# Performance work log

Hardware: AMD Instinct MI355X
Metric: run time of the kernel (lower is better)

## Reference

```python
import jax, jax.numpy as jnp
from jax import lax
import numpy as np


def _tv1d_row(y, lam):
    """Condat's direct O(n) 1D TV-L1 prox (TV1D_denoise) on one row.
    Solves min_x 0.5*||x-y||^2 + lam * sum|x_{i+1}-x_i|.
    State machine translation of Condat (2013) Algorithm 1.
    """
    W = y.shape[0]
    idx = jnp.arange(W)
    dt = y.dtype

    def write(out, lo, hi, v):
        # out[lo:hi+1] = v  (masked, jit-friendly)
        return jnp.where((idx >= lo) & (idx <= hi), v, out)

    def cond_fn(s):
        return ~s[9]

    def body_fn(s):
        out, k, k0, km, kp, umin, umax, vmin, vmax, done = s
        T = jnp.array(True)
        F = jnp.array(False)

        def branchA(_):  # k == W-1
            def a1(_):  # umin < 0: flush negative segment at vmin
                o = write(out, k0, km, vmin)
                k0n = km + 1
                vminn = y[jnp.minimum(k0n, W - 1)]
                return (o, k0n, k0n, k0n, kp, lam, vminn + lam - vmax, vminn, vmax, F)

            def a2(_):  # umax > 0: flush positive segment at vmax
                o = write(out, k0, kp, vmax)
                k0n = kp + 1
                vmaxn = y[jnp.minimum(k0n, W - 1)]
                return (o, k0n, k0n, km, k0n, vmaxn - lam - vmin, -lam, vmin, vmaxn, F)

            def a3(_):  # terminate
                v = vmin + umin / (k - k0 + 1).astype(dt)
                o = write(out, k0, k, v)
                return (o, k, k0, km, kp, umin, umax, v, vmax, T)

            return lax.cond(umin < 0, a1,
                            lambda _: lax.cond(umax > 0, a2, a3, None), None)

        def branchB(_):  # k < W-1
            yn = y[jnp.minimum(k + 1, W - 1)]
            umin_t = umin + yn - vmin
            umax_t = umax + yn - vmax

            def b1(_):  # negative jump: flush at vmin, restart
                o = write(out, k0, km, vmin)
                k0n = km + 1
                vminn = y[jnp.minimum(k0n, W - 1)]
                return (o, k0n, k0n, k0n, k0n, lam, -lam, vminn, vminn + 2 * lam, F)

            def b2(_):  # positive jump: flush at vmax, restart
                o = write(out, k0, kp, vmax)
                k0n = kp + 1
                vmaxn = y[jnp.minimum(k0n, W - 1)]
                return (o, k0n, k0n, k0n, k0n, lam, -lam, vmaxn - 2 * lam, vmaxn, F)

            def b3(_):  # extend current segment
                kn = k + 1
                denom = (kn - k0 + 1).astype(dt)
                hit_min = umin_t >= lam
                hit_max = umax_t <= -lam
                vminn = jnp.where(hit_min, vmin + (umin_t - lam) / denom, vmin)
                uminn = jnp.where(hit_min, lam, umin_t)
                kmn = jnp.where(hit_min, kn, km)
                vmaxn = jnp.where(hit_max, vmax + (umax_t + lam) / denom, vmax)
                umaxn = jnp.where(hit_max, -lam, umax_t)
                kpn = jnp.where(hit_max, kn, kp)
                return (out, kn, k0, kmn, kpn, uminn, umaxn, vminn, vmaxn, F)

            return lax.cond(umin_t < -lam, b1,
                            lambda _: lax.cond(umax_t > lam, b2, b3, None), None)

        return lax.cond(k == W - 1, branchA, branchB, None)

    z = jnp.int32(0)
    init = (jnp.zeros_like(y), z, z, z, z, lam, -lam, y[0] - lam, y[0] + lam, jnp.array(False))
    return lax.while_loop(cond_fn, body_fn, init)[0]


def tv1d_batch(y_flat, lam_rows):
    return jax.vmap(_tv1d_row)(y_flat, lam_rows)


def setup_inputs() -> dict:
    key = jax.random.key(0)
    N, C, H, W = 8, 3, 256, 512
    y = jax.random.normal(key, (N, C, H, W), dtype=jnp.float32)
    # learned lmbd parameter initialized so that softplus(lmbd) = 0.5 (lmbd_init=0.5, lmbd_zero<0 -> offset 0)
    lmbd = jnp.full((1, C), float(np.log(np.expm1(0.5))), dtype=jnp.float32)
    return {"y": y, "lmbd": lmbd}


def reference(y, lmbd):
    N, C, H, W = y.shape
    lam = jax.nn.softplus(lmbd)  # get_lmbd_val with lmbd_offset = 0
    lam_rows = jnp.broadcast_to(lam.reshape(1, C, 1), (N, C, H)).reshape(-1)  # (N*C*H,)
    x = tv1d_batch(y.reshape(-1, W), lam_rows)
    return x.reshape(N, C, H, W)
```

## Files before the change

### kernel.cpp

```cpp
#include <hip/hip_runtime.h>
#include <math.h>

#define TVW 512
#define TVH 256
#define TVC 3
#define WPB 2
#define BLOCK (WPB * 64)
#define PAD 12
#define RTN 528

__global__ __launch_bounds__(BLOCK)
void tv1d_condat_wave_kernel(const float* __restrict__ y,
                             const float* __restrict__ lmbd,
                             float* __restrict__ out,
                             int total_rows) {
    __shared__ __align__(16) float buf [WPB * TVW + PAD];
    __shared__ __align__(16) float bneg[WPB * TVW + PAD];
    __shared__ __align__(16) float rtab[RTN];
    const int tid  = threadIdx.x;
    const int wave = tid >> 6;
    const int lane = tid & 63;
    const int l32  = lane & 31;
    const bool hi  = lane >= 32;
    const int row  = blockIdx.x * WPB + wave;

    if (row < total_rows) {
        const float4* s4 = (const float4*)(y + (size_t)row * TVW);
        float4* b4 = (float4*)(buf  + wave * TVW);
        float4* n4 = (float4*)(bneg + wave * TVW);
        #pragma unroll
        for (int i = 0; i < TVW / 4; i += 64) {
            const float4 vv = s4[i + lane];
            b4[i + lane] = vv;
            n4[i + lane] = make_float4(-vv.x, -vv.y, -vv.z, -vv.w);
        }
    }
    if (tid < PAD) {
        buf [WPB * TVW + tid] = 0.0f;
        bneg[WPB * TVW + tid] = 0.0f;
    }
    for (int i = tid; i < RTN; i += BLOCK)
        rtab[i] = 1.0f / (float)(i == 0 ? 1 : i);
    __syncthreads();

    if (row < total_rows) {
        const int c = (row / TVH) % TVC;
        float lam = log1pf(expf(lmbd[c]));
        lam = __uint_as_float(__builtin_amdgcn_readfirstlane(__float_as_uint(lam)));
        const float nlam   = -lam;
        const float twolam = 2.0f * lam;
        float* x = buf + wave * TVW;
        const float* xs = hi ? (bneg + wave * TVW) : (buf + wave * TVW);
        const float cneg = hi ? twolam : 0.0f;
        const float cpos = hi ? 0.0f : twolam;

        int k0, t, trips, rem, seg_guard;
        int kmv, kcv;
        unsigned long long jb;
        float u, v, nv, tt, wv, den_f;
        float P0, P1, P2, P3, Q0, Q1, Q2, Q3, R0, R1, R2, R3, e0, e1, e2;
        float2 TAr, TBr, TAp, TBp, TAq, TBq;
        const float* rt;
        bool negj;

        k0 = 0; seg_guard = 2048; jb = 0;
        kmv = 0; kcv = 1;
        v = xs[0] - lam;
        u = lam;
        P0 = xs[1];  P1 = xs[2];  P2 = xs[3];  P3 = xs[4];
        Q0 = xs[5];  Q1 = xs[6];  Q2 = xs[7];  Q3 = xs[8];
        R0 = xs[9];  R1 = xs[10]; R2 = xs[11]; R3 = xs[12];

#define TVSTEP(EV, RN) { \
            const float u_t = u + (EV) - v; \
            jb = __ballot(u_t < nlam);    \
            if (jb) goto midjump; \
            kmv = (u_t >= lam) ? kcv : kmv;   \
            kcv += 1; \
            const float u_n = fminf(u_t, lam); \
            v = fmaf(u_t - u_n, (RN), v);   \
            u = u_n; }

#define TVPHASE(B0_, B1_, B2_, B3_, TA_, TB_) { \
            TVSTEP(B0_, TA_.x) \
            TVSTEP(B1_, TA_.y) \
            TVSTEP(B2_, TB_.x) \
            TVSTEP(B3_, TB_.y) \
            B0_ = xs[k0 + t + 13]; B1_ = xs[k0 + t + 14]; \
            B2_ = xs[k0 + t + 15]; B3_ = xs[k0 + t + 16]; \
            TA_ = *(const float2*)(rt + 12); \
            TB_ = *(const float2*)(rt + 14); \
            rt += 4; t += 4; }

seg_start:
        if (--seg_guard < 0) goto done;
        trips = (TVW - 1) - k0;
        TAr = *(const float2*)(rtab + 10); TBr = *(const float2*)(rtab + 12);
        TAp = *(const float2*)(rtab + 14); TBp = *(const float2*)(rtab + 16);
        TAq = *(const float2*)(rtab + 18); TBq = *(const float2*)(rtab + 20);
        if (trips < 4) { t = 0; e0 = P0; e1 = P1; e2 = P2; goto rem_steps; }
        TVSTEP(P0, 0.5f)
        TVSTEP(P1, (1.0f / 3.0f))
        TVSTEP(P2, 0.25f)
        TVSTEP(P3, 0.2f)
        P0 = xs[k0 + 13]; P1 = xs[k0 + 14]; P2 = xs[k0 + 15]; P3 = xs[k0 + 16];
        if (trips < 8) { t = 4; e0 = Q0; e1 = Q1; e2 = Q2; goto rem_steps; }
        TVSTEP(Q0, (1.0f / 6.0f))
        TVSTEP(Q1, (1.0f / 7.0f))
        TVSTEP(Q2, 0.125f)
        TVSTEP(Q3, (1.0f / 9.0f))
        Q0 = xs[k0 + 17]; Q1 = xs[k0 + 18]; Q2 = xs[k0 + 19]; Q3 = xs[k0 + 20];
        t = 8;
        rt = rtab + 10;
        for (;;) {
            if (t + 4 > trips) { e0 = R0; e1 = R1; e2 = R2; break; }
            TVPHASE(R0, R1, R2, R3, TAr, TBr)
            if (t + 4 > trips) { e0 = P0; e1 = P1; e2 = P2; break; }
            TVPHASE(P0, P1, P2, P3, TAp, TBp)
            if (t + 4 > trips) { e0 = Q0; e1 = Q1; e2 = Q2; break; }
            TVPHASE(Q0, Q1, Q2, Q3, TAq, TBq)
        }
rem_steps:
        rem = trips - t;
        if (rem > 0) {
            den_f = (float)(t + 2);
            TVSTEP(e0, __builtin_amdgcn_rcpf(den_f))
            if (rem > 1) {
                TVSTEP(e1, __builtin_amdgcn_rcpf(den_f + 1.0f))
                if (rem > 2) {
                    TVSTEP(e2, __builtin_amdgcn_rcpf(den_f + 2.0f))
                }
            }
        }

        {
            const unsigned long long bb = __ballot(u < 0.0f);
            if ((unsigned)bb) {
                const int fe = __builtin_amdgcn_readlane(kmv, 0);
                const int k0n = fe + 1;
                wv = v;
                if (k0n < TVW) {
                    nv = xs[k0n];
                    P0 = xs[k0n + 1];  P1 = xs[k0n + 2];  P2 = xs[k0n + 3];  P3 = xs[k0n + 4];
                    Q0 = xs[k0n + 5];  Q1 = xs[k0n + 6];  Q2 = xs[k0n + 7];  Q3 = xs[k0n + 8];
                    R0 = xs[k0n + 9];  R1 = xs[k0n + 10]; R2 = xs[k0n + 11]; R3 = xs[k0n + 12];
                }
                { const int pe = fe < TVW - 1 ? fe : TVW - 1;
                  if (!hi) for (int p = k0 + l32; p <= pe; p += 32) x[p] = wv; }
                if (k0n >= TVW) goto done;
                tt = nv - lam;
                u = hi ? (tt - v) : lam;
                v = hi ? v : nv;
                k0 = k0n;
                kmv = hi ? kmv : k0n;
                kcv = k0n + 1;
                goto seg_start;
            } else if ((unsigned)(bb >> 32)) {
                const int fe = __builtin_amdgcn_readlane(kmv, 32);
                const int k0n = fe + 1;
                wv = -v;
                if (k0n < TVW) {
                    nv = xs[k0n];
                    P0 = xs[k0n + 1];  P1 = xs[k0n + 2];  P2 = xs[k0n + 3];  P3 = xs[k0n + 4];
                    Q0 = xs[k0n + 5];  Q1 = xs[k0n + 6];  Q2 = xs[k0n + 7];  Q3 = xs[k0n + 8];
                    R0 = xs[k0n + 9];  R1 = xs[k0n + 10]; R2 = xs[k0n + 11]; R3 = xs[k0n + 12];
                }
                { const int pe = fe < TVW - 1 ? fe : TVW - 1;
                  if (hi) for (int p = k0 + l32; p <= pe; p += 32) x[p] = wv; }
                if (k0n >= TVW) goto done;
                tt = nv - lam;
                u = hi ? lam : (tt - v);
                v = hi ? nv : v;
                k0 = k0n;
                kmv = hi ? k0n : kmv;
                kcv = k0n + 1;
                goto seg_start;
            } else {
                const float vt = fmaf(u, __builtin_amdgcn_rcpf((float)(trips + 1)), v);
                if (!hi) for (int p = k0 + l32; p < TVW; p += 32) x[p] = vt;
                goto done;
            }
        }

midjump:
        {
            negj = (unsigned)jb != 0;
            const int fe = __builtin_amdgcn_readlane(kmv, negj ? 0 : 32);
            const int k0n = fe + 1;
            wv = hi ? -v : v;
            nv = xs[k0n];
            P0 = xs[k0n + 1];  P1 = xs[k0n + 2];  P2 = xs[k0n + 3];  P3 = xs[k0n + 4];
            Q0 = xs[k0n + 5];  Q1 = xs[k0n + 6];  Q2 = xs[k0n + 7];  Q3 = xs[k0n + 8];
            R0 = xs[k0n + 9];  R1 = xs[k0n + 10]; R2 = xs[k0n + 11]; R3 = xs[k0n + 12];
            {
                const int p0 = k0 + l32;
                if ((negj != hi) && (p0 <= fe)) x[p0] = wv;
                if (fe - k0 >= 32) {
                    if (negj != hi)
                        for (int p = p0 + 32; p <= fe; p += 32) x[p] = wv;
                }
            }
            k0 = k0n;
            kmv = k0n; kcv = k0n + 1;
            v = nv - (negj ? cneg : cpos);
            u = lam;
            goto seg_start;
        }
#undef TVPHASE
#undef TVSTEP
done:   ;
        {
            const float4* b4 = (const float4*)(buf + wave * TVW);
            float4* d4 = (float4*)(out + (size_t)row * TVW);
            #pragma unroll
            for (int i = 0; i < TVW / 4; i += 64)
                d4[i + lane] = b4[i + lane];
        }
    }
}

extern "C" void kernel_launch(void* const* d_in, const int* in_sizes, int n_in,
                              void* d_out, int out_size, void* d_ws, size_t ws_size,
                              hipStream_t stream) {
    const float* y    = (const float*)d_in[0];
    const float* lmbd = (const float*)d_in[1];
    float* out = (float*)d_out;

    const int total_rows = in_sizes[0] / TVW;
    const int grid = (total_rows + WPB - 1) / WPB;
    tv1d_condat_wave_kernel<<<grid, BLOCK, 0, stream>>>(y, lmbd, out, total_rows);
}
```

Baseline: 236.6 us.

## Keep row data and reciprocals in VGPR windows read via readlane instead of LDS

Each wave now holds a sliding 64-element window of the row, plus a second window, in registers. Per-step values y[k] and 1/(k+1) come from v_readlane instead of LDS loads. The negated copy buffer and the reciprocal table in shared memory are removed. The upper half-wave's sign flip is folded into an fma with a per-lane sign, and reciprocals are computed per lane with rcp. This aims to cut LDS traffic and load latency on the serial dependency chain, but it adds readlane to SGPR moves and window-slide reloads that also sit on that chain.

```diff
diff --git a/kernel.cpp b/kernel.cpp
--- a/kernel.cpp
+++ b/kernel.cpp
@@ -6,17 +6,14 @@
 #define TVC 3
 #define WPB 2
 #define BLOCK (WPB * 64)
-#define PAD 12
-#define RTN 528
+#define PADF 128
 
 __global__ __launch_bounds__(BLOCK)
 void tv1d_condat_wave_kernel(const float* __restrict__ y,
                              const float* __restrict__ lmbd,
                              float* __restrict__ out,
                              int total_rows) {
-    __shared__ __align__(16) float buf [WPB * TVW + PAD];
-    __shared__ __align__(16) float bneg[WPB * TVW + PAD];
-    __shared__ __align__(16) float rtab[RTN];
+    __shared__ __align__(16) float buf[WPB * TVW + PADF];
     const int tid  = threadIdx.x;
     const int wave = tid >> 6;
     const int lane = tid & 63;
@@ -24,113 +21,106 @@
     const bool hi  = lane >= 32;
     const int row  = blockIdx.x * WPB + wave;
 
+#define RLF(SRC, IDX) __uint_as_float(__builtin_amdgcn_readlane(__float_as_uint(SRC), (IDX)))
+
     if (row < total_rows) {
-        const float4* s4 = (const float4*)(y + (size_t)row * TVW);
-        float4* b4 = (float4*)(buf  + wave * TVW);
-        float4* n4 = (float4*)(bneg + wave * TVW);
-        #pragma unroll
-        for (int i = 0; i < TVW / 4; i += 64) {
-            const float4 vv = s4[i + lane];
-            b4[i + lane] = vv;
-            n4[i + lane] = make_float4(-vv.x, -vv.y, -vv.z, -vv.w);
-        }
-    }
-    if (tid < PAD) {
-        buf [WPB * TVW + tid] = 0.0f;
-        bneg[WPB * TVW + tid] = 0.0f;
-    }
-    for (int i = tid; i < RTN; i += BLOCK)
-        rtab[i] = 1.0f / (float)(i == 0 ? 1 : i);
-    __syncthreads();
-
-    if (row < total_rows) {
+        {
+            const float4* s4 = (const float4*)(y + (size_t)row * TVW);
+            float4* b4 = (float4*)(buf + wave * TVW);
+            #pragma unroll
+            for (int i = 0; i < TVW / 4; i += 64)
+                b4[i + lane] = s4[i + lane];
+        }
+
         const int c = (row / TVH) % TVC;
         float lam = log1pf(expf(lmbd[c]));
         lam = __uint_as_float(__builtin_amdgcn_readfirstlane(__float_as_uint(lam)));
         const float nlam   = -lam;
         const float twolam = 2.0f * lam;
         float* x = buf + wave * TVW;
-        const float* xs = hi ? (bneg + wave * TVW) : (buf + wave * TVW);
-        const float cneg = hi ? twolam : 0.0f;
-        const float cpos = hi ? 0.0f : twolam;
-
-        int k0, t, trips, rem, seg_guard;
-        int kmv, kcv;
+
+        const float sgn   = hi ? -1.0f : 1.0f;
+        const float vnlam = -lam;
+        const float vmcn  = hi ? -twolam : -0.0f;
+        const float vmcp  = hi ? -0.0f : -twolam;
+        const float laneF = (float)lane;
+        const float rw0c  = __builtin_amdgcn_rcpf(laneF + 1.0f);
+        const float rw1c  = __builtin_amdgcn_rcpf(laneF + 57.0f);
+
+        int k0, wb, trips, trips_rel, s_ji, seg_guard, kmv, kcv;
         unsigned long long jb;
-        float u, v, nv, tt, wv, den_f;
-        float P0, P1, P2, P3, Q0, Q1, Q2, Q3, R0, R1, R2, R3, e0, e1, e2;
-        float2 TAr, TBr, TAp, TBp, TAq, TBq;
-        const float* rt;
+        float u, v, nvs, wv, tt, denbF, rwin, rwin2, ywin, ywin2;
         bool negj;
 
-        k0 = 0; seg_guard = 2048; jb = 0;
+        k0 = 0; seg_guard = 4096; jb = 0;
+        ywin  = x[lane];
+        ywin2 = x[56 + lane];
+        nvs = RLF(ywin, 0);
+        v = fmaf(sgn, nvs, vnlam);
+        u = lam;
         kmv = 0; kcv = 1;
-        v = xs[0] - lam;
-        u = lam;
-        P0 = xs[1];  P1 = xs[2];  P2 = xs[3];  P3 = xs[4];
-        Q0 = xs[5];  Q1 = xs[6];  Q2 = xs[7];  Q3 = xs[8];
-        R0 = xs[9];  R1 = xs[10]; R2 = xs[11]; R3 = xs[12];
-
-#define TVSTEP(EV, RN) { \
-            const float u_t = u + (EV) - v; \
+
+#define TVSTEP(SY, SR) { \
+            const float u_t = fmaf(sgn, (SY), u) - v; \
             jb = __ballot(u_t < nlam);    \
             if (jb) goto midjump; \
             kmv = (u_t >= lam) ? kcv : kmv;   \
             kcv += 1; \
             const float u_n = fminf(u_t, lam); \
-            v = fmaf(u_t - u_n, (RN), v);   \
+            v = fmaf(u_t - u_n, (SR), v);     \
             u = u_n; }
 
-#define TVPHASE(B0_, B1_, B2_, B3_, TA_, TB_) { \
-            TVSTEP(B0_, TA_.x) \
-            TVSTEP(B1_, TA_.y) \
-            TVSTEP(B2_, TB_.x) \
-            TVSTEP(B3_, TB_.y) \
-            B0_ = xs[k0 + t + 13]; B1_ = xs[k0 + t + 14]; \
-            B2_ = xs[k0 + t + 15]; B3_ = xs[k0 + t + 16]; \
-            TA_ = *(const float2*)(rt + 12); \
-            TB_ = *(const float2*)(rt + 14); \
-            rt += 4; t += 4; }
+#define TVSLIDE() { \
+            ywin = ywin2; \
+            wb += 56; \
+            ywin2 = x[wb + 56 + lane]; \
+            s_ji -= 56; trips_rel -= 56; \
+            rwin = rwin2; \
+            rwin2 = __builtin_amdgcn_rcpf(laneF + denbF); \
+            denbF += 56.0f; }
 
 seg_start:
         if (--seg_guard < 0) goto done;
         trips = (TVW - 1) - k0;
-        TAr = *(const float2*)(rtab + 10); TBr = *(const float2*)(rtab + 12);
-        TAp = *(const float2*)(rtab + 14); TBp = *(const float2*)(rtab + 16);
-        TAq = *(const float2*)(rtab + 18); TBq = *(const float2*)(rtab + 20);
-        if (trips < 4) { t = 0; e0 = P0; e1 = P1; e2 = P2; goto rem_steps; }
-        TVSTEP(P0, 0.5f)
-        TVSTEP(P1, (1.0f / 3.0f))
-        TVSTEP(P2, 0.25f)
-        TVSTEP(P3, 0.2f)
-        P0 = xs[k0 + 13]; P1 = xs[k0 + 14]; P2 = xs[k0 + 15]; P3 = xs[k0 + 16];
-        if (trips < 8) { t = 4; e0 = Q0; e1 = Q1; e2 = Q2; goto rem_steps; }
-        TVSTEP(Q0, (1.0f / 6.0f))
-        TVSTEP(Q1, (1.0f / 7.0f))
-        TVSTEP(Q2, 0.125f)
-        TVSTEP(Q3, (1.0f / 9.0f))
-        Q0 = xs[k0 + 17]; Q1 = xs[k0 + 18]; Q2 = xs[k0 + 19]; Q3 = xs[k0 + 20];
-        t = 8;
-        rt = rtab + 10;
-        for (;;) {
-            if (t + 4 > trips) { e0 = R0; e1 = R1; e2 = R2; break; }
-            TVPHASE(R0, R1, R2, R3, TAr, TBr)
-            if (t + 4 > trips) { e0 = P0; e1 = P1; e2 = P2; break; }
-            TVPHASE(P0, P1, P2, P3, TAp, TBp)
-            if (t + 4 > trips) { e0 = Q0; e1 = Q1; e2 = Q2; break; }
-            TVPHASE(Q0, Q1, Q2, Q3, TAq, TBq)
-        }
-rem_steps:
-        rem = trips - t;
-        if (rem > 0) {
-            den_f = (float)(t + 2);
-            TVSTEP(e0, __builtin_amdgcn_rcpf(den_f))
-            if (rem > 1) {
-                TVSTEP(e1, __builtin_amdgcn_rcpf(den_f + 1.0f))
-                if (rem > 2) {
-                    TVSTEP(e2, __builtin_amdgcn_rcpf(den_f + 2.0f))
-                }
+        trips_rel = trips;
+        wb = k0;
+        s_ji = 1;
+        denbF = 113.0f;
+        rwin = rw0c; rwin2 = rw1c;
+        if (trips >= 8) {
+            TVSTEP(RLF(ywin, 1), 0.5f)
+            TVSTEP(RLF(ywin, 2), (1.0f / 3.0f))
+            TVSTEP(RLF(ywin, 3), 0.25f)
+            TVSTEP(RLF(ywin, 4), 0.2f)
+            TVSTEP(RLF(ywin, 5), (1.0f / 6.0f))
+            TVSTEP(RLF(ywin, 6), (1.0f / 7.0f))
+            TVSTEP(RLF(ywin, 7), 0.125f)
+            TVSTEP(RLF(ywin, 8), (1.0f / 9.0f))
+            s_ji = 9;
+            for (;;) {
+                if (s_ji + 7 > trips_rel) break;
+                if (s_ji > 56) TVSLIDE()
+                {
+                    const int j0 = s_ji,     j1 = s_ji + 1, j2 = s_ji + 2, j3 = s_ji + 3,
+                              j4 = s_ji + 4, j5 = s_ji + 5, j6 = s_ji + 6, j7 = s_ji + 7;
+                    const float y0 = RLF(ywin, j0), y1 = RLF(ywin, j1),
+                                y2 = RLF(ywin, j2), y3 = RLF(ywin, j3),
+                                y4 = RLF(ywin, j4), y5 = RLF(ywin, j5),
+                                y6 = RLF(ywin, j6), y7 = RLF(ywin, j7);
+                    const float r0 = RLF(rwin, j0), r1 = RLF(rwin, j1),
+                                r2 = RLF(rwin, j2), r3 = RLF(rwin, j3),
+                                r4 = RLF(rwin, j4), r5 = RLF(rwin, j5),
+                                r6 = RLF(rwin, j6), r7 = RLF(rwin, j7);
+                    TVSTEP(y0, r0) TVSTEP(y1, r1) TVSTEP(y2, r2) TVSTEP(y3, r3)
+                    TVSTEP(y4, r4) TVSTEP(y5, r5) TVSTEP(y6, r6) TVSTEP(y7, r7)
+                }
+                s_ji += 8;
             }
+        }
+        while (s_ji <= trips_rel) {
+            if (s_ji > 63) TVSLIDE()
+            TVSTEP(RLF(ywin, s_ji), RLF(rwin, s_ji))
+            s_ji += 1;
         }
 
         {
@@ -140,40 +130,38 @@
                 const int k0n = fe + 1;
                 wv = v;
                 if (k0n < TVW) {
-                    nv = xs[k0n];
-                    P0 = xs[k0n + 1];  P1 = xs[k0n + 2];  P2 = xs[k0n + 3];  P3 = xs[k0n + 4];
-                    Q0 = xs[k0n + 5];  Q1 = xs[k0n + 6];  Q2 = xs[k0n + 7];  Q3 = xs[k0n + 8];
-                    R0 = xs[k0n + 9];  R1 = xs[k0n + 10]; R2 = xs[k0n + 11]; R3 = xs[k0n + 12];
+                    ywin  = x[k0n + lane];
+                    ywin2 = x[k0n + 56 + lane];
                 }
                 { const int pe = fe < TVW - 1 ? fe : TVW - 1;
                   if (!hi) for (int p = k0 + l32; p <= pe; p += 32) x[p] = wv; }
                 if (k0n >= TVW) goto done;
-                tt = nv - lam;
+                nvs = RLF(ywin, 0);
+                tt = fmaf(sgn, nvs, vnlam);
                 u = hi ? (tt - v) : lam;
-                v = hi ? v : nv;
-                k0 = k0n;
+                v = hi ? v : nvs;
                 kmv = hi ? kmv : k0n;
                 kcv = k0n + 1;
+                k0 = k0n;
                 goto seg_start;
             } else if ((unsigned)(bb >> 32)) {
                 const int fe = __builtin_amdgcn_readlane(kmv, 32);
                 const int k0n = fe + 1;
                 wv = -v;
                 if (k0n < TVW) {
-                    nv = xs[k0n];
-                    P0 = xs[k0n + 1];  P1 = xs[k0n + 2];  P2 = xs[k0n + 3];  P3 = xs[k0n + 4];
-                    Q0 = xs[k0n + 5];  Q1 = xs[k0n + 6];  Q2 = xs[k0n + 7];  Q3 = xs[k0n + 8];
-                    R0 = xs[k0n + 9];  R1 = xs[k0n + 10]; R2 = xs[k0n + 11]; R3 = xs[k0n + 12];
+                    ywin  = x[k0n + lane];
+                    ywin2 = x[k0n + 56 + lane];
                 }
                 { const int pe = fe < TVW - 1 ? fe : TVW - 1;
                   if (hi) for (int p = k0 + l32; p <= pe; p += 32) x[p] = wv; }
                 if (k0n >= TVW) goto done;
-                tt = nv - lam;
+                nvs = RLF(ywin, 0);
+                tt = nvs + vnlam;
                 u = hi ? lam : (tt - v);
-                v = hi ? nv : v;
-                k0 = k0n;
+                v = hi ? (-nvs) : v;
                 kmv = hi ? k0n : kmv;
                 kcv = k0n + 1;
+                k0 = k0n;
                 goto seg_start;
             } else {
                 const float vt = fmaf(u, __builtin_amdgcn_rcpf((float)(trips + 1)), v);
@@ -188,10 +176,8 @@
             const int fe = __builtin_amdgcn_readlane(kmv, negj ? 0 : 32);
             const int k0n = fe + 1;
             wv = hi ? -v : v;
-            nv = xs[k0n];
-            P0 = xs[k0n + 1];  P1 = xs[k0n + 2];  P2 = xs[k0n + 3];  P3 = xs[k0n + 4];
-            Q0 = xs[k0n + 5];  Q1 = xs[k0n + 6];  Q2 = xs[k0n + 7];  Q3 = xs[k0n + 8];
-            R0 = xs[k0n + 9];  R1 = xs[k0n + 10]; R2 = xs[k0n + 11]; R3 = xs[k0n + 12];
+            ywin  = x[k0n + lane];
+            ywin2 = x[k0n + 56 + lane];
             {
                 const int p0 = k0 + l32;
                 if ((negj != hi) && (p0 <= fe)) x[p0] = wv;
@@ -200,14 +186,15 @@
                         for (int p = p0 + 32; p <= fe; p += 32) x[p] = wv;
                 }
             }
+            nvs = RLF(ywin, 0);
+            v = fmaf(sgn, nvs, negj ? vmcn : vmcp);
+            u = lam;
+            kmv = k0n; kcv = k0n + 1;
             k0 = k0n;
-            kmv = k0n; kcv = k0n + 1;
-            v = nv - (negj ? cneg : cpos);
-            u = lam;
             goto seg_start;
         }
-#undef TVPHASE
 #undef TVSTEP
+#undef TVSLIDE
 done:   ;
         {
             const float4* b4 = (const float4*)(buf + wave * TVW);
@@ -217,6 +204,7 @@
                 d4[i + lane] = b4[i + lane];
         }
     }
+#undef RLF
 }
 
 extern "C" void kernel_launch(void* const* d_in, const int* in_sizes, int n_in,
```

Result: slower. 243.7 us (+3.0%).
